# Performance work log

Measured on AMD Instinct MI355X. Metric: run time of the kernel, lower is better.

## Reference

```python
import jax, jax.numpy as jnp
import numpy as np

T, B, X, Y = 24, 16, 64, 64
S, M, C = 16, 8, 8
F = S + M + C   # GRU input_size = 32
H = 32          # hidden_size


def setup_inputs() -> dict:
    key = jax.random.key(0)
    ks = jax.random.split(key, 8)
    inv = 1.0 / np.sqrt(H)
    return {
        "spatial": jax.random.normal(ks[0], (T, B, X, Y, S), dtype=jnp.float32),
        "meteorology": jax.random.normal(ks[1], (T, B, X, Y, M), dtype=jnp.float32),
        "context": jax.random.normal(ks[2], (T, B, X, Y, C), dtype=jnp.float32),
        # GRU parameters (torch layout: [3H, F] and [3H, H], gate order r,z,n)
        "W_ih": jax.random.uniform(ks[3], (3 * H, F), jnp.float32, -inv, inv),
        "W_hh": jax.random.uniform(ks[4], (3 * H, H), jnp.float32, -inv, inv),
        "b_ih": jax.random.uniform(ks[5], (3 * H,), jnp.float32, -inv, inv),
        "b_hh": jax.random.uniform(ks[6], (3 * H,), jnp.float32, -inv, inv),
        # output projection (hidden -> spatial_size)
        "W": jax.random.normal(ks[7], (H, S), dtype=jnp.float32),
    }


def reference(spatial, meteorology, context, W_ih, W_hh, b_ih, b_hh, W):
    # cat features: (T, B, X, Y, F); merge all pixels + batch into one GRU batch
    x = jnp.concatenate((spatial, meteorology, context), axis=4)
    N = B * X * Y
    x = x.reshape(T, N, F)

    # precompute input projections for all timesteps: (T, N, 3H)
    gx_all = jnp.einsum('tnf,gf->tng', x, W_ih) + b_ih

    def step(h, gx):
        gh = h @ W_hh.T + b_hh                      # (N, 3H)
        r = jax.nn.sigmoid(gx[:, :H] + gh[:, :H])
        z = jax.nn.sigmoid(gx[:, H:2 * H] + gh[:, H:2 * H])
        n = jnp.tanh(gx[:, 2 * H:] + r * gh[:, 2 * H:])
        h = (1.0 - z) * n + z * h
        return h, None

    h0 = jnp.zeros((N, H), dtype=x.dtype)
    h_final, _ = jax.lax.scan(step, h0, gx_all)     # (N, H)

    out = h_final @ W                               # (N, S)
    return out.reshape(B, X, Y, S)
```

## Files before the change

kernel.cpp:

```cpp
#include <hip/hip_runtime.h>


#define TSTEPS 24
#define NPIX 65536
#define PADW 40

typedef __attribute__((ext_vector_type(8))) short bf16x8;
typedef __attribute__((ext_vector_type(4))) float f32x4;
typedef __attribute__((ext_vector_type(4))) unsigned int u32x4;

#define MFMA16(a, b, c) __builtin_amdgcn_mfma_f32_16x16x32_bf16((a), (b), (c), 0, 0, 0)

__device__ __forceinline__ unsigned short f2bf(float f) {
  unsigned u = __builtin_bit_cast(unsigned, f);
  u += 0x7fffu + ((u >> 16) & 1u);
  return (unsigned short)(u >> 16);
}

__device__ __forceinline__ unsigned pk2(float a, float b) {
  unsigned ua = __builtin_bit_cast(unsigned, a);
  unsigned ub = __builtin_bit_cast(unsigned, b);
  ua += 0x7fffu + ((ua >> 16) & 1u);
  ub += 0x7fffu + ((ub >> 16) & 1u);
  return __builtin_amdgcn_perm(ub, ua, 0x07060302u);
}

__device__ __forceinline__ bf16x8 pack8(f32x4 a, f32x4 b) {
  u32x4 r = { pk2(a[0], a[1]), pk2(a[2], a[3]), pk2(b[0], b[1]), pk2(b[2], b[3]) };
  return __builtin_bit_cast(bf16x8, r);
}

__device__ __forceinline__ float sigmoid_(float x) {
  return __builtin_amdgcn_rcpf(1.f + __expf(-x));
}
__device__ __forceinline__ float tanh_(float x) {
  return 1.f - 2.f * __builtin_amdgcn_rcpf(__expf(2.f * x) + 1.f);
}

__device__ __forceinline__ bf16x8 relayout_h(const f32x4 h0, const f32x4 h1, int lane) {
  unsigned p00 = pk2(h0[0], h0[1]), p01 = pk2(h0[2], h0[3]);
  unsigned p10 = pk2(h1[0], h1[1]), p11 = pk2(h1[2], h1[3]);
  const int lo = (lane & 15) | ((lane & 16) << 1);
  const int hi = lo + 16;
  unsigned a0 = (unsigned)__shfl((int)p00, lo, 64);
  unsigned a1 = (unsigned)__shfl((int)p01, lo, 64);
  unsigned a2 = (unsigned)__shfl((int)p00, hi, 64);
  unsigned a3 = (unsigned)__shfl((int)p01, hi, 64);
  unsigned b0 = (unsigned)__shfl((int)p10, lo, 64);
  unsigned b1 = (unsigned)__shfl((int)p11, lo, 64);
  unsigned b2 = (unsigned)__shfl((int)p10, hi, 64);
  unsigned b3 = (unsigned)__shfl((int)p11, hi, 64);
  const bool t1 = (lane & 32) != 0;
  u32x4 d = { t1 ? b0 : a0, t1 ? b1 : a1, t1 ? b2 : a2, t1 ? b3 : a3 };
  return __builtin_bit_cast(bf16x8, d);
}

__global__ __launch_bounds__(256, 4)
void gru_fused(const float* __restrict__ spatial, const float* __restrict__ met,
               const float* __restrict__ ctx,
               const float* __restrict__ W_ih, const float* __restrict__ W_hh,
               const float* __restrict__ b_ih, const float* __restrict__ b_hh,
               const float* __restrict__ Wout, float* __restrict__ out) {
  __shared__ __align__(16) unsigned short sWih[96 * PADW];

  const int tid = threadIdx.x;
  for (int i = tid; i < 96 * 32; i += 256) {
    int r = i >> 5, c = i & 31;
    sWih[r * PADW + c] = f2bf(W_ih[i]);
  }
  __syncthreads();

  const int lane = tid & 63;
  const int col = lane & 15;
  const int q = lane >> 4;
  const int wave = blockIdx.x * 4 + (tid >> 6);
  const long p = (long)wave * 16 + col;

  bf16x8 whh[6];
#pragma unroll
  for (int i = 0; i < 6; ++i) {
    const float* wp = W_hh + (i * 16 + col) * 32 + q * 8;
    whh[i] = pack8(*(const f32x4*)wp, *(const f32x4*)(wp + 4));
  }
  f32x4 cS[4];
#pragma unroll
  for (int i = 0; i < 4; ++i)
    cS[i] = *(const f32x4*)&b_ih[i * 16 + q * 4] + *(const f32x4*)&b_hh[i * 16 + q * 4];
  const f32x4 cG4 = *(const f32x4*)&b_ih[64 + q * 4];
  const f32x4 cG5 = *(const f32x4*)&b_ih[80 + q * 4];
  const f32x4 cH4 = *(const f32x4*)&b_hh[64 + q * 4];
  const f32x4 cH5 = *(const f32x4*)&b_hh[80 + q * 4];

  const float* xptr;
  long xstride;
  if (q < 2)       { xptr = spatial + p * 16 + q * 8; xstride = (long)NPIX * 16; }
  else if (q == 2) { xptr = met + p * 8;              xstride = (long)NPIX * 8;  }
  else             { xptr = ctx + p * 8;              xstride = (long)NPIX * 8;  }

  bf16x8 bx = pack8(*(const f32x4*)xptr, *(const f32x4*)(xptr + 4));
  xptr += xstride;

  f32x4 h0 = {0.f, 0.f, 0.f, 0.f};
  f32x4 h1 = {0.f, 0.f, 0.f, 0.f};

#pragma unroll 1
  for (int t = 0; t < TSTEPS; ++t) {
    f32x4 xna, xnb;
    if (t < TSTEPS - 1) {
      xna = *(const f32x4*)xptr;
      xnb = *(const f32x4*)(xptr + 4);
      xptr += xstride;
    }

    bf16x8 bh = relayout_h(h0, h1, lane);

    const int wb = col * PADW + q * 8;
    bf16x8 a0 = *(const bf16x8*)&sWih[wb];
    bf16x8 a1 = *(const bf16x8*)&sWih[wb + 16 * PADW];
    bf16x8 a2 = *(const bf16x8*)&sWih[wb + 32 * PADW];
    bf16x8 a3 = *(const bf16x8*)&sWih[wb + 48 * PADW];
    bf16x8 a4 = *(const bf16x8*)&sWih[wb + 64 * PADW];
    bf16x8 a5 = *(const bf16x8*)&sWih[wb + 80 * PADW];

    f32x4 g0 = MFMA16(a0, bx, cS[0]);
    f32x4 g1 = MFMA16(a1, bx, cS[1]);
    f32x4 g2 = MFMA16(a2, bx, cS[2]);
    f32x4 g3 = MFMA16(a3, bx, cS[3]);
    f32x4 G4 = MFMA16(a4, bx, cG4);
    f32x4 G5 = MFMA16(a5, bx, cG5);
    f32x4 S0 = MFMA16(whh[0], bh, g0);
    f32x4 S1 = MFMA16(whh[1], bh, g1);
    f32x4 S2 = MFMA16(whh[2], bh, g2);
    f32x4 S3 = MFMA16(whh[3], bh, g3);
    f32x4 H4 = MFMA16(whh[4], bh, cH4);
    f32x4 H5 = MFMA16(whh[5], bh, cH5);

#pragma unroll
    for (int r = 0; r < 4; ++r) {
      float rv0 = sigmoid_(S0[r]);
      float rv1 = sigmoid_(S1[r]);
      float zv0 = sigmoid_(S2[r]);
      float zv1 = sigmoid_(S3[r]);
      float nv0 = tanh_(G4[r] + rv0 * H4[r]);
      float nv1 = tanh_(G5[r] + rv1 * H5[r]);
      h0[r] = nv0 + zv0 * (h0[r] - nv0);
      h1[r] = nv1 + zv1 * (h1[r] - nv1);
    }

    if (t < TSTEPS - 1) bx = pack8(xna, xnb);
  }

  bf16x8 bhf = relayout_h(h0, h1, lane);
  float w[8];
#pragma unroll
  for (int j = 0; j < 8; ++j) w[j] = Wout[(q * 8 + j) * 16 + col];
  u32x4 awp = { pk2(w[0], w[1]), pk2(w[2], w[3]), pk2(w[4], w[5]), pk2(w[6], w[7]) };
  bf16x8 aw = __builtin_bit_cast(bf16x8, awp);
  const f32x4 zero = {0.f, 0.f, 0.f, 0.f};
  f32x4 o = MFMA16(aw, bhf, zero);
  *(f32x4*)&out[p * 16 + q * 4] = o;
}

extern "C" void kernel_launch(void* const* d_in, const int* in_sizes, int n_in,
                              void* d_out, int out_size, void* d_ws, size_t ws_size,
                              hipStream_t stream) {
  const float* spatial = (const float*)d_in[0];
  const float* met     = (const float*)d_in[1];
  const float* ctx     = (const float*)d_in[2];
  const float* W_ih    = (const float*)d_in[3];
  const float* W_hh    = (const float*)d_in[4];
  const float* b_ih    = (const float*)d_in[5];
  const float* b_hh    = (const float*)d_in[6];
  const float* Wout    = (const float*)d_in[7];
  float* out = (float*)d_out;

  gru_fused<<<dim3(NPIX / 16 / 4), dim3(256), 0, stream>>>(
      spatial, met, ctx, W_ih, W_hh, b_ih, b_hh, Wout, out);
}
```

Measured before the change: 283.3 us.

## Stage W_hh and biases in LDS, unroll time loop by two

```diff
diff --git a/kernel.cpp b/kernel.cpp
--- a/kernel.cpp
+++ b/kernel.cpp
@@ -1,4 +1,5 @@
 #include <hip/hip_runtime.h>
+#include <hip/hip_bf16.h>
 
 
 #define TSTEPS 24
@@ -18,11 +19,10 @@
 }
 
 __device__ __forceinline__ unsigned pk2(float a, float b) {
-  unsigned ua = __builtin_bit_cast(unsigned, a);
-  unsigned ub = __builtin_bit_cast(unsigned, b);
-  ua += 0x7fffu + ((ua >> 16) & 1u);
-  ub += 0x7fffu + ((ub >> 16) & 1u);
-  return __builtin_amdgcn_perm(ub, ua, 0x07060302u);
+  __hip_bfloat162 h = __float22bfloat162_rn(float2{a, b});
+  unsigned u;
+  __builtin_memcpy(&u, &h, sizeof(u));
+  return u;
 }
 
 __device__ __forceinline__ bf16x8 pack8(f32x4 a, f32x4 b) {
@@ -61,13 +61,20 @@
                const float* __restrict__ W_ih, const float* __restrict__ W_hh,
                const float* __restrict__ b_ih, const float* __restrict__ b_hh,
                const float* __restrict__ Wout, float* __restrict__ out) {
-  __shared__ __align__(16) unsigned short sWih[96 * PADW];
+  __shared__ __align__(16) unsigned short sW[192 * PADW];
+  __shared__ __align__(16) float sCB[64];
+  __shared__ __align__(16) float sBIN[32];
+  __shared__ __align__(16) float sBHN[32];
 
   const int tid = threadIdx.x;
   for (int i = tid; i < 96 * 32; i += 256) {
     int r = i >> 5, c = i & 31;
-    sWih[r * PADW + c] = f2bf(W_ih[i]);
+    sW[r * PADW + c] = f2bf(W_ih[i]);
+    sW[(96 + r) * PADW + c] = f2bf(W_hh[i]);
   }
+  if (tid < 64) sCB[tid] = b_ih[tid] + b_hh[tid];
+  else if (tid < 96) sBIN[tid - 64] = b_ih[tid];
+  else if (tid < 128) sBHN[tid - 96] = b_hh[tid - 32];
   __syncthreads();
 
   const int lane = tid & 63;
@@ -76,20 +83,13 @@
   const int wave = blockIdx.x * 4 + (tid >> 6);
   const long p = (long)wave * 16 + col;
 
-  bf16x8 whh[6];
-#pragma unroll
-  for (int i = 0; i < 6; ++i) {
-    const float* wp = W_hh + (i * 16 + col) * 32 + q * 8;
-    whh[i] = pack8(*(const f32x4*)wp, *(const f32x4*)(wp + 4));
-  }
   f32x4 cS[4];
 #pragma unroll
-  for (int i = 0; i < 4; ++i)
-    cS[i] = *(const f32x4*)&b_ih[i * 16 + q * 4] + *(const f32x4*)&b_hh[i * 16 + q * 4];
-  const f32x4 cG4 = *(const f32x4*)&b_ih[64 + q * 4];
-  const f32x4 cG5 = *(const f32x4*)&b_ih[80 + q * 4];
-  const f32x4 cH4 = *(const f32x4*)&b_hh[64 + q * 4];
-  const f32x4 cH5 = *(const f32x4*)&b_hh[80 + q * 4];
+  for (int i = 0; i < 4; ++i) cS[i] = *(const f32x4*)&sCB[i * 16 + q * 4];
+  const f32x4 cG4 = *(const f32x4*)&sBIN[q * 4];
+  const f32x4 cG5 = *(const f32x4*)&sBIN[16 + q * 4];
+  const f32x4 cH4 = *(const f32x4*)&sBHN[q * 4];
+  const f32x4 cH5 = *(const f32x4*)&sBHN[16 + q * 4];
 
   const float* xptr;
   long xstride;
@@ -103,7 +103,9 @@
   f32x4 h0 = {0.f, 0.f, 0.f, 0.f};
   f32x4 h1 = {0.f, 0.f, 0.f, 0.f};
 
-#pragma unroll 1
+  const int wb = col * PADW + q * 8;
+
+#pragma unroll 2
   for (int t = 0; t < TSTEPS; ++t) {
     f32x4 xna, xnb;
     if (t < TSTEPS - 1) {
@@ -114,13 +116,18 @@
 
     bf16x8 bh = relayout_h(h0, h1, lane);
 
-    const int wb = col * PADW + q * 8;
-    bf16x8 a0 = *(const bf16x8*)&sWih[wb];
-    bf16x8 a1 = *(const bf16x8*)&sWih[wb + 16 * PADW];
-    bf16x8 a2 = *(const bf16x8*)&sWih[wb + 32 * PADW];
-    bf16x8 a3 = *(const bf16x8*)&sWih[wb + 48 * PADW];
-    bf16x8 a4 = *(const bf16x8*)&sWih[wb + 64 * PADW];
-    bf16x8 a5 = *(const bf16x8*)&sWih[wb + 80 * PADW];
+    bf16x8 a0 = *(const bf16x8*)&sW[wb];
+    bf16x8 a1 = *(const bf16x8*)&sW[wb + 16 * PADW];
+    bf16x8 a2 = *(const bf16x8*)&sW[wb + 32 * PADW];
+    bf16x8 a3 = *(const bf16x8*)&sW[wb + 48 * PADW];
+    bf16x8 a4 = *(const bf16x8*)&sW[wb + 64 * PADW];
+    bf16x8 a5 = *(const bf16x8*)&sW[wb + 80 * PADW];
+    bf16x8 w0 = *(const bf16x8*)&sW[wb + 96 * PADW];
+    bf16x8 w1 = *(const bf16x8*)&sW[wb + 112 * PADW];
+    bf16x8 w2 = *(const bf16x8*)&sW[wb + 128 * PADW];
+    bf16x8 w3 = *(const bf16x8*)&sW[wb + 144 * PADW];
+    bf16x8 w4 = *(const bf16x8*)&sW[wb + 160 * PADW];
+    bf16x8 w5 = *(const bf16x8*)&sW[wb + 176 * PADW];
 
     f32x4 g0 = MFMA16(a0, bx, cS[0]);
     f32x4 g1 = MFMA16(a1, bx, cS[1]);
@@ -128,12 +135,12 @@
     f32x4 g3 = MFMA16(a3, bx, cS[3]);
     f32x4 G4 = MFMA16(a4, bx, cG4);
     f32x4 G5 = MFMA16(a5, bx, cG5);
-    f32x4 S0 = MFMA16(whh[0], bh, g0);
-    f32x4 S1 = MFMA16(whh[1], bh, g1);
-    f32x4 S2 = MFMA16(whh[2], bh, g2);
-    f32x4 S3 = MFMA16(whh[3], bh, g3);
-    f32x4 H4 = MFMA16(whh[4], bh, cH4);
-    f32x4 H5 = MFMA16(whh[5], bh, cH5);
+    f32x4 S0 = MFMA16(w0, bh, g0);
+    f32x4 S1 = MFMA16(w1, bh, g1);
+    f32x4 S2 = MFMA16(w2, bh, g2);
+    f32x4 S3 = MFMA16(w3, bh, g3);
+    f32x4 H4 = MFMA16(w4, bh, cH4);
+    f32x4 H5 = MFMA16(w5, bh, cH5);
 
 #pragma unroll
     for (int r = 0; r < 4; ++r) {
```

Result: no change. 279.4 us (-1.4%).
